# Performance work log

Hardware: AMD Instinct MI355X
Metric: run time of the kernel (lower is better)

Reference implementation:

```python
import jax, jax.numpy as jnp
import numpy as np

NUM_HEADS = 16
D_MODEL = 1024


def setup_inputs() -> dict:
    key = jax.random.key(0)
    ks = jax.random.split(key, 12)
    B, S, D = 2, 2048, D_MODEL
    scale = 1.0 / np.sqrt(D)
    inp = {
        "query": jax.random.normal(ks[0], (B, S, D), dtype=jnp.float32),
        "key": jax.random.normal(ks[1], (B, S, D), dtype=jnp.float32),
        "value": jax.random.normal(ks[2], (B, S, D), dtype=jnp.float32),
        "mask": jax.random.randint(ks[3], (B, S, S), 0, 2, dtype=jnp.int32),
        # four Linear(d_model, d_model) layers: torch layout W [out, in], y = x @ W.T + b
        "Wq": jax.random.normal(ks[4], (D, D), dtype=jnp.float32) * scale,
        "bq": jnp.zeros((D,), dtype=jnp.float32),
        "Wk": jax.random.normal(ks[5], (D, D), dtype=jnp.float32) * scale,
        "bk": jnp.zeros((D,), dtype=jnp.float32),
        "Wv": jax.random.normal(ks[6], (D, D), dtype=jnp.float32) * scale,
        "bv": jnp.zeros((D,), dtype=jnp.float32),
        "Wo": jax.random.normal(ks[7], (D, D), dtype=jnp.float32) * scale,
        "bo": jnp.zeros((D,), dtype=jnp.float32),
    }
    return inp


def reference(query, key, value, mask, Wq, bq, Wk, bk, Wv, bv, Wo, bo):
    B, S, D = query.shape
    H = NUM_HEADS
    dk = D // H

    def split_heads(x):  # [B,S,D] -> [B,H,S,dk]
        return x.reshape(B, S, H, dk).transpose(0, 2, 1, 3)

    q = split_heads(query @ Wq.T + bq)
    k = split_heads(key @ Wk.T + bk)
    v = split_heads(value @ Wv.T + bv)

    # naive full-score attention, faithful to the original
    scores = jnp.einsum("bhqd,bhkd->bhqk", q, k) / jnp.sqrt(jnp.asarray(dk, q.dtype))
    scores = jnp.where(mask[:, None, :, :] == 0, jnp.asarray(-1e9, scores.dtype), scores)
    probs = jax.nn.softmax(scores, axis=-1)
    attn = jnp.einsum("bhqk,bhkd->bhqd", probs, v)  # [B,H,S,dk]

    out = attn.transpose(0, 2, 1, 3).reshape(B, S, D)
    return out @ Wo.T + bo
```

## Files before the change

### kernel.cpp

```cpp
#include <hip/hip_runtime.h>
#include <hip/hip_bf16.h>

#define NH 16
#define DK 64
#define SEQ 2048
#define DMODEL 1024
#define BATCH 2
#define MROWS (BATCH * SEQ)

using bf16x8 = __attribute__((ext_vector_type(8))) short;
using f32x4  = __attribute__((ext_vector_type(4))) float;

#define NEGI (-1e30f)
#define QSCALE 0.18033688f

static __device__ __forceinline__ unsigned short f2bf(float x) {
  unsigned u = __builtin_bit_cast(unsigned, x);
  u += 0x7fffu + ((u >> 16) & 1u);
  return (unsigned short)(u >> 16);
}
static __device__ __forceinline__ float bf2f(unsigned short h) {
  unsigned u = ((unsigned)h) << 16;
  return __builtin_bit_cast(float, u);
}
static __device__ __forceinline__ unsigned cvtpk(float a, float b) {
  unsigned r;
  asm("v_cvt_pk_bf16_f32 %0, %1, %2" : "=v"(r) : "v"(a), "v"(b));
  return r;
}
static __device__ __forceinline__ void gl_lds16(const unsigned short* g,
                                                unsigned short* l) {
  __builtin_amdgcn_global_load_lds(
      (const __attribute__((address_space(1))) unsigned int*)g,
      (__attribute__((address_space(3))) unsigned int*)l, 16, 0, 0);
}

__global__ __launch_bounds__(256) void convert3(const float* __restrict__ s0,
                                                const float* __restrict__ s1,
                                                const float* __restrict__ s2,
                                                unsigned short* __restrict__ d0,
                                                unsigned short* __restrict__ d1,
                                                unsigned short* __restrict__ d2,
                                                long n8, int blkseg) {
  int seg = blockIdx.x / blkseg;
  int ib  = blockIdx.x % blkseg;
  const float* s = seg == 0 ? s0 : (seg == 1 ? s1 : s2);
  unsigned short* d = seg == 0 ? d0 : (seg == 1 ? d1 : d2);
  long i0 = (long)ib * blockDim.x + threadIdx.x;
  long stride = (long)blkseg * blockDim.x;
  for (long i = i0; i < n8; i += stride) {
    const float* p = s + i * 8;
    float4 a = *(const float4*)(p);
    float4 b = *(const float4*)(p + 4);
    uint4 u = {cvtpk(a.x, a.y), cvtpk(a.z, a.w), cvtpk(b.x, b.y), cvtpk(b.z, b.w)};
    *(bf16x8*)(d + i * 8) = __builtin_bit_cast(bf16x8, u);
  }
}
__global__ __launch_bounds__(256) void convert4(const float* __restrict__ s0,
                                                const float* __restrict__ s1,
                                                const float* __restrict__ s2,
                                                const float* __restrict__ s3,
                                                unsigned short* __restrict__ d0,
                                                unsigned short* __restrict__ d1,
                                                unsigned short* __restrict__ d2,
                                                unsigned short* __restrict__ d3,
                                                long n8, int blkseg) {
  int seg = blockIdx.x / blkseg;
  int ib  = blockIdx.x % blkseg;
  const float* s = seg == 0 ? s0 : (seg == 1 ? s1 : (seg == 2 ? s2 : s3));
  unsigned short* d = seg == 0 ? d0 : (seg == 1 ? d1 : (seg == 2 ? d2 : d3));
  long i0 = (long)ib * blockDim.x + threadIdx.x;
  long stride = (long)blkseg * blockDim.x;
  for (long i = i0; i < n8; i += stride) {
    const float* p = s + i * 8;
    float4 a = *(const float4*)(p);
    float4 b = *(const float4*)(p + 4);
    uint4 u = {cvtpk(a.x, a.y), cvtpk(a.z, a.w), cvtpk(b.x, b.y), cvtpk(b.z, b.w)};
    *(bf16x8*)(d + i * 8) = __builtin_bit_cast(bf16x8, u);
  }
}

__global__ __launch_bounds__(256) void pack_mask(const int* __restrict__ mask,
                                                 unsigned long long* __restrict__ pm,
                                                 int nwords) {
  int wid  = (blockIdx.x * blockDim.x + threadIdx.x) >> 6;
  int lane = threadIdx.x & 63;
  int nw   = (gridDim.x * blockDim.x) >> 6;
  for (int w = wid; w < nwords; w += nw) {
    int v = mask[(long)w * 64 + lane];
    unsigned long long b = __ballot(v != 0);
    if (lane == 0) pm[w] = b;
  }
}

#define BK 32

static __device__ __forceinline__ void gemm_body(const unsigned short* __restrict__ A,
                                                 const unsigned short* __restrict__ W,
                                                 const unsigned short* __restrict__ bias,
                                                 void* __restrict__ Cv,
                                                 int mode, float cscale, int bid,
                                                 unsigned short* Al, unsigned short* Bl) {
  const int t    = threadIdx.x;
  const int lane = t & 63;
  const int w    = t >> 6;
  const int wm   = w >> 1, wn = w & 1;
  const int g    = lane >> 4, lr = lane & 15;
  const int nb   = bid & 7;
  const int mb   = bid >> 3;
  const long Abase = (long)mb * 128 * 1024;
  const long Wbase = (long)nb * 128 * 1024;
  const int srow = lane >> 2;
  const int scol = (lane & 3) << 3;

  f32x4 acc[4][4] = {};

  for (int kt = 0; kt < 1024; kt += BK) {
    __syncthreads();
#pragma unroll
    for (int q = 0; q < 2; ++q) {
      int slab = w * 2 + q;
      int row  = slab * 16 + srow;
      gl_lds16(A + Abase + (long)row * 1024 + kt + scol, Al + slab * 512);
      gl_lds16(W + Wbase + (long)row * 1024 + kt + scol, Bl + slab * 512);
    }
    asm volatile("s_waitcnt vmcnt(0)" ::: "memory");
    __syncthreads();
    bf16x8 af[4], bfr[4];
#pragma unroll
    for (int i = 0; i < 4; ++i) {
      af[i]  = *(const bf16x8*)(&Al[(wm * 64 + i * 16 + lr) * 32 + g * 8]);
      bfr[i] = *(const bf16x8*)(&Bl[(wn * 64 + i * 16 + lr) * 32 + g * 8]);
    }
#pragma unroll
    for (int i = 0; i < 4; ++i)
#pragma unroll
      for (int j = 0; j < 4; ++j)
        acc[i][j] = __builtin_amdgcn_mfma_f32_16x16x32_bf16(af[i], bfr[j], acc[i][j], 0, 0, 0);
  }

#pragma unroll
  for (int j = 0; j < 4; ++j) {
    int n = nb * 128 + wn * 64 + j * 16 + lr;
    float bv = bf2f(bias[n]);
#pragma unroll
    for (int i = 0; i < 4; ++i) {
      int m0 = mb * 128 + wm * 64 + i * 16 + g * 4;
      float v0 = (acc[i][j][0] + bv) * cscale;
      float v1 = (acc[i][j][1] + bv) * cscale;
      float v2 = (acc[i][j][2] + bv) * cscale;
      float v3 = (acc[i][j][3] + bv) * cscale;
      if (mode == 2) {
        int b = m0 >> 11, s0 = m0 & (SEQ - 1);
        int h = n >> 6, d = n & (DK - 1);
        uint2 pk;
        pk.x = (unsigned)f2bf(v0) | ((unsigned)f2bf(v1) << 16);
        pk.y = (unsigned)f2bf(v2) | ((unsigned)f2bf(v3) << 16);
        *(uint2*)(&((unsigned short*)Cv)[((long)(b * NH + h) * DK + d) * SEQ + s0]) = pk;
      } else if (mode == 1) {
        int b = m0 >> 11, s0 = m0 & (SEQ - 1);
        int h = n >> 6, d = n & (DK - 1);
        unsigned short* p = &((unsigned short*)Cv)[(((long)(b * NH + h) * SEQ + s0) << 6) + d];
        p[0] = f2bf(v0); p[64] = f2bf(v1); p[128] = f2bf(v2); p[192] = f2bf(v3);
      } else {
        float* p = &((float*)Cv)[(long)m0 * DMODEL + n];
        p[0] = v0; p[DMODEL] = v1; p[2 * DMODEL] = v2; p[3 * DMODEL] = v3;
      }
    }
  }
}

__global__ __launch_bounds__(256) void qkv_proj(const unsigned short* __restrict__ Aq,
                                                const unsigned short* __restrict__ Ak,
                                                const unsigned short* __restrict__ Av,
                                                const unsigned short* __restrict__ Wq,
                                                const unsigned short* __restrict__ Wk,
                                                const unsigned short* __restrict__ Wv,
                                                const unsigned short* __restrict__ bq,
                                                const unsigned short* __restrict__ bk,
                                                const unsigned short* __restrict__ bv,
                                                unsigned short* __restrict__ Cq,
                                                unsigned short* __restrict__ Ck,
                                                unsigned short* __restrict__ Cv) {
  __shared__ unsigned short Al[128 * 32];
  __shared__ unsigned short Bl[128 * 32];
  int which = blockIdx.x >> 8;
  int bid   = blockIdx.x & 255;
  const unsigned short* A = which == 0 ? Aq : (which == 1 ? Ak : Av);
  const unsigned short* W = which == 0 ? Wq : (which == 1 ? Wk : Wv);
  const unsigned short* b = which == 0 ? bq : (which == 1 ? bk : bv);
  unsigned short* C = which == 0 ? Cq : (which == 1 ? Ck : Cv);
  int   mode  = which == 2 ? 2 : 1;
  float scale = which == 0 ? QSCALE : 1.0f;
  gemm_body(A, W, b, C, mode, scale, bid, Al, Bl);
}

__global__ __launch_bounds__(256) void gemm_out(const unsigned short* __restrict__ A,
                                                const unsigned short* __restrict__ W,
                                                const unsigned short* __restrict__ bias,
                                                float* __restrict__ C) {
  __shared__ unsigned short Al[128 * 32];
  __shared__ unsigned short Bl[128 * 32];
  gemm_body(A, W, bias, C, 0, 1.0f, blockIdx.x, Al, Bl);
}

#define KVB 64
#define LD 72

__global__ __launch_bounds__(256) void attn(const unsigned short* __restrict__ Q,
                                            const unsigned short* __restrict__ K,
                                            const unsigned short* __restrict__ VT,
                                            const unsigned long long* __restrict__ pm,
                                            unsigned short* __restrict__ O) {
  __shared__ unsigned short Kl[KVB * LD];
  __shared__ unsigned short Vt[DK * LD];
  __shared__ unsigned short Pl[4][32 * LD];
  const int t    = threadIdx.x;
  const int lane = t & 63;
  const int w    = t >> 6;
  const int g    = lane >> 4, lr = lane & 15;
  const int bh   = blockIdx.x & 31;
  const int qb   = blockIdx.x >> 5;
  const int b    = bh >> 4, h = bh & 15;
  const long base = (long)bh * SEQ * DK;
  const int q0   = qb * 128 + w * 32;

  const int kr0 = t >> 3,         kc0 = (t & 7) << 3;
  const int kr1 = (256 + t) >> 3, kc1 = kc0;

  bf16x8 qf[2][2];
#pragma unroll
  for (int qh = 0; qh < 2; ++qh) {
    const unsigned short* qp = Q + base + (long)(q0 + qh * 16 + lr) * DK;
    qf[qh][0] = *(const bf16x8*)(qp + g * 8);
    qf[qh][1] = *(const bf16x8*)(qp + 32 + g * 8);
  }
  float mrun[2] = {NEGI, NEGI}, lrun[2] = {0.f, 0.f};
  f32x4 o[2][4] = {};

  bf16x8 kreg0 = *(const bf16x8*)(K + base + (long)kr0 * DK + kc0);
  bf16x8 kreg1 = *(const bf16x8*)(K + base + (long)kr1 * DK + kc1);
  bf16x8 vreg0 = *(const bf16x8*)(VT + base + (long)kr0 * SEQ + kc0);
  bf16x8 vreg1 = *(const bf16x8*)(VT + base + (long)kr1 * SEQ + kc1);

  for (int kt = 0; kt < SEQ / KVB; ++kt) {
    __syncthreads();
    *(bf16x8*)(&Kl[kr0 * LD + kc0]) = kreg0;
    *(bf16x8*)(&Kl[kr1 * LD + kc1]) = kreg1;
    *(bf16x8*)(&Vt[kr0 * LD + kc0]) = vreg0;
    *(bf16x8*)(&Vt[kr1 * LD + kc1]) = vreg1;
    if (kt + 1 < SEQ / KVB) {
      const int kvb = (kt + 1) * KVB;
      kreg0 = *(const bf16x8*)(K + base + (long)(kvb + kr0) * DK + kc0);
      kreg1 = *(const bf16x8*)(K + base + (long)(kvb + kr1) * DK + kc1);
      vreg0 = *(const bf16x8*)(VT + base + (long)kr0 * SEQ + kvb + kc0);
      vreg1 = *(const bf16x8*)(VT + base + (long)kr1 * SEQ + kvb + kc1);
    }
    __syncthreads();

    f32x4 sc[2][4];
#pragma unroll
    for (int c = 0; c < 4; ++c) {
      bf16x8 kf0 = *(const bf16x8*)(&Kl[(c * 16 + lr) * LD + g * 8]);
      bf16x8 kf1 = *(const bf16x8*)(&Kl[(c * 16 + lr) * LD + 32 + g * 8]);
#pragma unroll
      for (int qh = 0; qh < 2; ++qh) {
        f32x4 a = {};
        a = __builtin_amdgcn_mfma_f32_16x16x32_bf16(kf0, qf[qh][0], a, 0, 0, 0);
        a = __builtin_amdgcn_mfma_f32_16x16x32_bf16(kf1, qf[qh][1], a, 0, 0, 0);
        sc[qh][c] = a;
      }
    }

    unsigned short* P = &Pl[w][0];
#pragma unroll
    for (int qh = 0; qh < 2; ++qh) {
      const unsigned long long mw = pm[((long)b * SEQ + q0 + qh * 16 + lr) * 32 + kt];
      float s[4][4];
      float mt = NEGI;
#pragma unroll
      for (int c = 0; c < 4; ++c)
#pragma unroll
        for (int r = 0; r < 4; ++r) {
          int kvi = c * 16 + g * 4 + r;
          float v = ((mw >> kvi) & 1ull) ? sc[qh][c][r] : -1e9f;
          s[c][r] = v;
          mt = fmaxf(mt, v);
        }
      mt = fmaxf(mt, __shfl_xor(mt, 16, 64));
      mt = fmaxf(mt, __shfl_xor(mt, 32, 64));

      int need = __any(mt > mrun[qh] + 5.0f);
      float mn = mrun[qh], corr = 1.0f;
      if (need) { mn = fmaxf(mrun[qh], mt); corr = __builtin_amdgcn_exp2f(mrun[qh] - mn); mrun[qh] = mn; }

      float pf[4][4];
      float rs = 0.f;
#pragma unroll
      for (int c = 0; c < 4; ++c)
#pragma unroll
        for (int r = 0; r < 4; ++r) {
          float p_ = __builtin_amdgcn_exp2f(s[c][r] - mn);
          pf[c][r] = p_;
          rs += p_;
        }
      rs += __shfl_xor(rs, 16, 64);
      rs += __shfl_xor(rs, 32, 64);

      if (need) {
        lrun[qh] = lrun[qh] * corr + rs;
#pragma unroll
        for (int r = 0; r < 4; ++r) {
          float cq = __shfl(corr, (lane >> 4) * 4 + r, 64);
#pragma unroll
          for (int dt = 0; dt < 4; ++dt) o[qh][dt][r] *= cq;
        }
      } else {
        lrun[qh] += rs;
      }

#pragma unroll
      for (int c = 0; c < 4; ++c) {
        uint2 pk;
        pk.x = cvtpk(pf[c][0], pf[c][1]);
        pk.y = cvtpk(pf[c][2], pf[c][3]);
        *(uint2*)(&P[(qh * 16 + lr) * LD + c * 16 + g * 4]) = pk;
      }
    }
    asm volatile("s_waitcnt lgkmcnt(0)" ::: "memory");
    __builtin_amdgcn_sched_barrier(0);

#pragma unroll
    for (int c32 = 0; c32 < 2; ++c32) {
      bf16x8 pf0 = *(const bf16x8*)(&P[lr * LD + c32 * 32 + g * 8]);
      bf16x8 pf1 = *(const bf16x8*)(&P[(16 + lr) * LD + c32 * 32 + g * 8]);
#pragma unroll
      for (int dt = 0; dt < 4; ++dt) {
        bf16x8 vf = *(const bf16x8*)(&Vt[(dt * 16 + lr) * LD + c32 * 32 + g * 8]);
        o[0][dt] = __builtin_amdgcn_mfma_f32_16x16x32_bf16(pf0, vf, o[0][dt], 0, 0, 0);
        o[1][dt] = __builtin_amdgcn_mfma_f32_16x16x32_bf16(pf1, vf, o[1][dt], 0, 0, 0);
      }
    }
    asm volatile("s_waitcnt lgkmcnt(0)" ::: "memory");
    __builtin_amdgcn_sched_barrier(0);
  }
#pragma unroll
  for (int qh = 0; qh < 2; ++qh) {
    float inv = 1.0f / lrun[qh];
#pragma unroll
    for (int r = 0; r < 4; ++r) {
      float iq = __shfl(inv, (lane >> 4) * 4 + r, 64);
      int q = q0 + qh * 16 + g * 4 + r;
      unsigned short* op = O + ((long)(b * SEQ + q) * DMODEL) + h * DK;
#pragma unroll
      for (int dt = 0; dt < 4; ++dt) op[dt * 16 + lr] = f2bf(o[qh][dt][r] * iq);
    }
  }
}

extern "C" void kernel_launch(void* const* d_in, const int* in_sizes, int n_in,
                              void* d_out, int out_size, void* d_ws, size_t ws_size,
                              hipStream_t stream) {
  const int* maskp = (const int*)d_in[3];
  float* out = (float*)d_out;

  char* ws = (char*)d_ws;
  const long MB = 1 << 20;
  unsigned long long* pm = (unsigned long long*)ws;
  unsigned short* Qc  = (unsigned short*)(ws + 1 * MB);
  unsigned short* Kc  = (unsigned short*)(ws + 9 * MB);
  unsigned short* Vc  = (unsigned short*)(ws + 17 * MB);
  unsigned short* Wqc = (unsigned short*)(ws + 25 * MB);
  unsigned short* Wkc = (unsigned short*)(ws + 27 * MB);
  unsigned short* Wvc = (unsigned short*)(ws + 29 * MB);
  unsigned short* Woc = (unsigned short*)(ws + 31 * MB);
  unsigned short* bqc = (unsigned short*)(ws + 33 * MB);
  unsigned short* bkc = (unsigned short*)(ws + 33 * MB + 4096);
  unsigned short* bvc = (unsigned short*)(ws + 33 * MB + 8192);
  unsigned short* boc = (unsigned short*)(ws + 33 * MB + 12288);
  unsigned short* Qb  = (unsigned short*)(ws + 35 * MB);
  unsigned short* Kb  = (unsigned short*)(ws + 43 * MB);
  unsigned short* Vb  = (unsigned short*)(ws + 51 * MB);
  unsigned short* Ab  = (unsigned short*)(ws + 59 * MB);

  const long nQKV8 = (long)MROWS * DMODEL / 8;
  const long nW8   = (long)DMODEL * DMODEL / 8;
  convert3<<<1536, 256, 0, stream>>>((const float*)d_in[0], (const float*)d_in[1],
                                     (const float*)d_in[2], Qc, Kc, Vc, nQKV8, 512);
  convert4<<<512, 256, 0, stream>>>((const float*)d_in[4], (const float*)d_in[6],
                                    (const float*)d_in[8], (const float*)d_in[10],
                                    Wqc, Wkc, Wvc, Woc, nW8, 128);
  convert4<<<4, 256, 0, stream>>>((const float*)d_in[5], (const float*)d_in[7],
                                  (const float*)d_in[9], (const float*)d_in[11],
                                  bqc, bkc, bvc, boc, DMODEL / 8, 1);

  const int nwords = BATCH * SEQ * (SEQ / 64);
  pack_mask<<<512, 256, 0, stream>>>(maskp, pm, nwords);

  qkv_proj<<<768, 256, 0, stream>>>(Qc, Kc, Vc, Wqc, Wkc, Wvc,
                                    bqc, bkc, bvc, Qb, Kb, Vb);

  attn<<<BATCH * NH * (SEQ / 128), 256, 0, stream>>>(Qb, Kb, Vb, pm, Ab);

  gemm_out<<<256, 256, 0, stream>>>(Ab, Woc, boc, out);
}
```

Before: 182.9 us.

## Merge conversion and mask-packing kernels into one prep launch; double GEMM K-tile

Replaces the four preprocessing launches (activation, weight and bias conversion plus mask packing) with one prep kernel that dispatches on block index, removing launch gaps and letting the pieces run concurrently. The projection GEMMs also move from a 32-wide to a 64-wide K tile, halving the number of barrier and load-wait rounds per output tile. The cost is double the LDS per block, which may lower occupancy, and the unpadded 64-element LDS rows may cause more bank conflicts.

```diff
diff --git a/kernel.cpp b/kernel.cpp
--- a/kernel.cpp
+++ b/kernel.cpp
@@ -35,65 +35,77 @@
       (__attribute__((address_space(3))) unsigned int*)l, 16, 0, 0);
 }
 
-__global__ __launch_bounds__(256) void convert3(const float* __restrict__ s0,
-                                                const float* __restrict__ s1,
-                                                const float* __restrict__ s2,
-                                                unsigned short* __restrict__ d0,
-                                                unsigned short* __restrict__ d1,
-                                                unsigned short* __restrict__ d2,
-                                                long n8, int blkseg) {
-  int seg = blockIdx.x / blkseg;
-  int ib  = blockIdx.x % blkseg;
-  const float* s = seg == 0 ? s0 : (seg == 1 ? s1 : s2);
-  unsigned short* d = seg == 0 ? d0 : (seg == 1 ? d1 : d2);
-  long i0 = (long)ib * blockDim.x + threadIdx.x;
-  long stride = (long)blkseg * blockDim.x;
-  for (long i = i0; i < n8; i += stride) {
-    const float* p = s + i * 8;
-    float4 a = *(const float4*)(p);
-    float4 b = *(const float4*)(p + 4);
-    uint4 u = {cvtpk(a.x, a.y), cvtpk(a.z, a.w), cvtpk(b.x, b.y), cvtpk(b.z, b.w)};
-    *(bf16x8*)(d + i * 8) = __builtin_bit_cast(bf16x8, u);
-  }
-}
-__global__ __launch_bounds__(256) void convert4(const float* __restrict__ s0,
-                                                const float* __restrict__ s1,
-                                                const float* __restrict__ s2,
-                                                const float* __restrict__ s3,
-                                                unsigned short* __restrict__ d0,
-                                                unsigned short* __restrict__ d1,
-                                                unsigned short* __restrict__ d2,
-                                                unsigned short* __restrict__ d3,
-                                                long n8, int blkseg) {
-  int seg = blockIdx.x / blkseg;
-  int ib  = blockIdx.x % blkseg;
-  const float* s = seg == 0 ? s0 : (seg == 1 ? s1 : (seg == 2 ? s2 : s3));
-  unsigned short* d = seg == 0 ? d0 : (seg == 1 ? d1 : (seg == 2 ? d2 : d3));
-  long i0 = (long)ib * blockDim.x + threadIdx.x;
-  long stride = (long)blkseg * blockDim.x;
-  for (long i = i0; i < n8; i += stride) {
-    const float* p = s + i * 8;
-    float4 a = *(const float4*)(p);
-    float4 b = *(const float4*)(p + 4);
-    uint4 u = {cvtpk(a.x, a.y), cvtpk(a.z, a.w), cvtpk(b.x, b.y), cvtpk(b.z, b.w)};
-    *(bf16x8*)(d + i * 8) = __builtin_bit_cast(bf16x8, u);
-  }
-}
-
-__global__ __launch_bounds__(256) void pack_mask(const int* __restrict__ mask,
-                                                 unsigned long long* __restrict__ pm,
-                                                 int nwords) {
-  int wid  = (blockIdx.x * blockDim.x + threadIdx.x) >> 6;
-  int lane = threadIdx.x & 63;
-  int nw   = (gridDim.x * blockDim.x) >> 6;
-  for (int w = wid; w < nwords; w += nw) {
-    int v = mask[(long)w * 64 + lane];
-    unsigned long long b = __ballot(v != 0);
-    if (lane == 0) pm[w] = b;
-  }
-}
-
-#define BK 32
+static __device__ __forceinline__ void conv8(const float* s, unsigned short* d, long i) {
+  const float* p = s + i * 8;
+  float4 a = *(const float4*)(p);
+  float4 b = *(const float4*)(p + 4);
+  uint4 u = {cvtpk(a.x, a.y), cvtpk(a.z, a.w), cvtpk(b.x, b.y), cvtpk(b.z, b.w)};
+  *(bf16x8*)(d + i * 8) = __builtin_bit_cast(bf16x8, u);
+}
+
+__global__ __launch_bounds__(256) void prep(const float* __restrict__ q,
+                                            const float* __restrict__ k,
+                                            const float* __restrict__ v,
+                                            const float* __restrict__ wq,
+                                            const float* __restrict__ wk,
+                                            const float* __restrict__ wv,
+                                            const float* __restrict__ wo,
+                                            const float* __restrict__ bq,
+                                            const float* __restrict__ bk,
+                                            const float* __restrict__ bv,
+                                            const float* __restrict__ bo,
+                                            const int* __restrict__ mask,
+                                            unsigned short* __restrict__ Qc,
+                                            unsigned short* __restrict__ Kc,
+                                            unsigned short* __restrict__ Vc,
+                                            unsigned short* __restrict__ Wqc,
+                                            unsigned short* __restrict__ Wkc,
+                                            unsigned short* __restrict__ Wvc,
+                                            unsigned short* __restrict__ Woc,
+                                            unsigned short* __restrict__ bqc,
+                                            unsigned short* __restrict__ bkc,
+                                            unsigned short* __restrict__ bvc,
+                                            unsigned short* __restrict__ boc,
+                                            unsigned long long* __restrict__ pm) {
+  const int bid = blockIdx.x;
+  const int t   = threadIdx.x;
+  const long nQKV8 = (long)MROWS * DMODEL / 8;
+  const long nW8   = (long)DMODEL * DMODEL / 8;
+  if (bid < 1536) {
+    int seg = bid >> 9;
+    int ib  = bid & 511;
+    const float* s = seg == 0 ? q : (seg == 1 ? k : v);
+    unsigned short* d = seg == 0 ? Qc : (seg == 1 ? Kc : Vc);
+    long i0 = (long)ib * 256 + t;
+    for (long i = i0; i < nQKV8; i += 512 * 256) conv8(s, d, i);
+  } else if (bid < 2048) {
+    int seg = (bid - 1536) >> 7;
+    int ib  = (bid - 1536) & 127;
+    const float* s = seg == 0 ? wq : (seg == 1 ? wk : (seg == 2 ? wv : wo));
+    unsigned short* d = seg == 0 ? Wqc : (seg == 1 ? Wkc : (seg == 2 ? Wvc : Woc));
+    long i0 = (long)ib * 256 + t;
+    for (long i = i0; i < nW8; i += 128 * 256) conv8(s, d, i);
+  } else if (bid < 2560) {
+    const int nwords = BATCH * SEQ * (SEQ / 64);
+    int wid  = (((bid - 2048) << 8) + t) >> 6;
+    int lane = t & 63;
+    for (int w = wid; w < nwords; w += 2048) {
+      int mv = mask[(long)w * 64 + lane];
+      unsigned long long bb = __ballot(mv != 0);
+      if (lane == 0) pm[w] = bb;
+    }
+  } else {
+    for (int c = t; c < 512; c += 256) {
+      int seg = c >> 7;
+      long i  = c & 127;
+      const float* s = seg == 0 ? bq : (seg == 1 ? bk : (seg == 2 ? bv : bo));
+      unsigned short* d = seg == 0 ? bqc : (seg == 1 ? bkc : (seg == 2 ? bvc : boc));
+      conv8(s, d, i);
+    }
+  }
+}
+
+#define BK 64
 
 static __device__ __forceinline__ void gemm_body(const unsigned short* __restrict__ A,
                                                  const unsigned short* __restrict__ W,
@@ -110,33 +122,36 @@
   const int mb   = bid >> 3;
   const long Abase = (long)mb * 128 * 1024;
   const long Wbase = (long)nb * 128 * 1024;
-  const int srow = lane >> 2;
-  const int scol = (lane & 3) << 3;
+  const int srow = lane >> 3;
+  const int scol = (lane & 7) << 3;
 
   f32x4 acc[4][4] = {};
 
   for (int kt = 0; kt < 1024; kt += BK) {
     __syncthreads();
 #pragma unroll
-    for (int q = 0; q < 2; ++q) {
-      int slab = w * 2 + q;
-      int row  = slab * 16 + srow;
+    for (int qq = 0; qq < 4; ++qq) {
+      int slab = w * 4 + qq;
+      int row  = slab * 8 + srow;
       gl_lds16(A + Abase + (long)row * 1024 + kt + scol, Al + slab * 512);
       gl_lds16(W + Wbase + (long)row * 1024 + kt + scol, Bl + slab * 512);
     }
     asm volatile("s_waitcnt vmcnt(0)" ::: "memory");
     __syncthreads();
-    bf16x8 af[4], bfr[4];
-#pragma unroll
-    for (int i = 0; i < 4; ++i) {
-      af[i]  = *(const bf16x8*)(&Al[(wm * 64 + i * 16 + lr) * 32 + g * 8]);
-      bfr[i] = *(const bf16x8*)(&Bl[(wn * 64 + i * 16 + lr) * 32 + g * 8]);
-    }
-#pragma unroll
-    for (int i = 0; i < 4; ++i)
-#pragma unroll
-      for (int j = 0; j < 4; ++j)
-        acc[i][j] = __builtin_amdgcn_mfma_f32_16x16x32_bf16(af[i], bfr[j], acc[i][j], 0, 0, 0);
+#pragma unroll
+    for (int kh = 0; kh < 2; ++kh) {
+      bf16x8 af[4], bfr[4];
+#pragma unroll
+      for (int i = 0; i < 4; ++i) {
+        af[i]  = *(const bf16x8*)(&Al[(wm * 64 + i * 16 + lr) * 64 + kh * 32 + g * 8]);
+        bfr[i] = *(const bf16x8*)(&Bl[(wn * 64 + i * 16 + lr) * 64 + kh * 32 + g * 8]);
+      }
+#pragma unroll
+      for (int i = 0; i < 4; ++i)
+#pragma unroll
+        for (int j = 0; j < 4; ++j)
+          acc[i][j] = __builtin_amdgcn_mfma_f32_16x16x32_bf16(af[i], bfr[j], acc[i][j], 0, 0, 0);
+    }
   }
 
 #pragma unroll
@@ -182,8 +197,8 @@
                                                 unsigned short* __restrict__ Cq,
                                                 unsigned short* __restrict__ Ck,
                                                 unsigned short* __restrict__ Cv) {
-  __shared__ unsigned short Al[128 * 32];
-  __shared__ unsigned short Bl[128 * 32];
+  __shared__ unsigned short Al[128 * 64];
+  __shared__ unsigned short Bl[128 * 64];
   int which = blockIdx.x >> 8;
   int bid   = blockIdx.x & 255;
   const unsigned short* A = which == 0 ? Aq : (which == 1 ? Ak : Av);
@@ -199,8 +214,8 @@
                                                 const unsigned short* __restrict__ W,
                                                 const unsigned short* __restrict__ bias,
                                                 float* __restrict__ C) {
-  __shared__ unsigned short Al[128 * 32];
-  __shared__ unsigned short Bl[128 * 32];
+  __shared__ unsigned short Al[128 * 64];
+  __shared__ unsigned short Bl[128 * 64];
   gemm_body(A, W, bias, C, 0, 1.0f, blockIdx.x, Al, Bl);
 }
 
@@ -383,19 +398,15 @@
   unsigned short* Vb  = (unsigned short*)(ws + 51 * MB);
   unsigned short* Ab  = (unsigned short*)(ws + 59 * MB);
 
-  const long nQKV8 = (long)MROWS * DMODEL / 8;
-  const long nW8   = (long)DMODEL * DMODEL / 8;
-  convert3<<<1536, 256, 0, stream>>>((const float*)d_in[0], (const float*)d_in[1],
-                                     (const float*)d_in[2], Qc, Kc, Vc, nQKV8, 512);
-  convert4<<<512, 256, 0, stream>>>((const float*)d_in[4], (const float*)d_in[6],
-                                    (const float*)d_in[8], (const float*)d_in[10],
-                                    Wqc, Wkc, Wvc, Woc, nW8, 128);
-  convert4<<<4, 256, 0, stream>>>((const float*)d_in[5], (const float*)d_in[7],
-                                  (const float*)d_in[9], (const float*)d_in[11],
-                                  bqc, bkc, bvc, boc, DMODEL / 8, 1);
-
-  const int nwords = BATCH * SEQ * (SEQ / 64);
-  pack_mask<<<512, 256, 0, stream>>>(maskp, pm, nwords);
+  prep<<<2561, 256, 0, stream>>>((const float*)d_in[0], (const float*)d_in[1],
+                                 (const float*)d_in[2],
+                                 (const float*)d_in[4], (const float*)d_in[6],
+                                 (const float*)d_in[8], (const float*)d_in[10],
+                                 (const float*)d_in[5], (const float*)d_in[7],
+                                 (const float*)d_in[9], (const float*)d_in[11],
+                                 maskp,
+                                 Qc, Kc, Vc, Wqc, Wkc, Wvc, Woc,
+                                 bqc, bkc, bvc, boc, pm);
 
   qkv_proj<<<768, 256, 0, stream>>>(Qc, Kc, Vc, Wqc, Wkc, Wvc,
                                     bqc, bkc, bvc, Qb, Kb, Vb);
```

New measurement: 191.0 us. +4.4%, slower.
